# Kernel optimization log

Measured on AMD Instinct MI355X. Metric: run time of the kernel, lower is better.

Reference implementation:

```python
import jax, jax.numpy as jnp
import numpy as np

HIDDEN = 1024
HEADS = 16
HEAD_DIM = HIDDEN // HEADS  # 64


def setup_inputs() -> dict:
    key = jax.random.key(0)
    ks = jax.random.split(key, 5)
    B, S = 1, 4096
    inputs = jax.random.normal(ks[0], (B, S, HIDDEN), dtype=jnp.float32)
    # Xavier-uniform-ish init for square [out, in] weights (torch Linear layout)
    lim = float(np.sqrt(6.0 / (HIDDEN + HIDDEN)))
    def w(k):
        return jax.random.uniform(k, (HIDDEN, HIDDEN), jnp.float32, -lim, lim)
    return {
        "inputs": inputs,
        "Wq": w(ks[1]), "bq": jnp.zeros((HIDDEN,), jnp.float32),
        "Wk": w(ks[2]), "bk": jnp.zeros((HIDDEN,), jnp.float32),
        "Wv": w(ks[3]), "bv": jnp.zeros((HIDDEN,), jnp.float32),
        "Wo": w(ks[4]), "bo": jnp.zeros((HIDDEN,), jnp.float32),
    }


def reference(inputs, Wq, bq, Wk, bk, Wv, bv, Wo, bo):
    # Chunked online-softmax attention (causal_mask=False) is mathematically
    # identical to standard softmax multi-head attention.
    B, S, _ = inputs.shape
    def proj(W, b):
        # torch Linear: x @ W.T + b, then split heads -> [B, S, H, D]
        return (inputs @ W.T + b).reshape(B, S, HEADS, HEAD_DIM)
    q = proj(Wq, bq) / jnp.asarray(np.sqrt(HEAD_DIM), inputs.dtype)
    k = proj(Wk, bk)
    v = proj(Wv, bv)
    scores = jnp.einsum("bqhd,bkhd->bhqk", q, k)          # [B, H, S, S]
    attn = jax.nn.softmax(scores, axis=-1)
    ctx = jnp.einsum("bhqk,bkhd->bqhd", attn, v)           # [B, S, H, D]
    ctx = ctx.reshape(B, S, HIDDEN)
    return ctx @ Wo.T + bo
```

## Files before the change

### kernel.cpp

```cpp
#include <hip/hip_runtime.h>
#include <hip/hip_bf16.h>

typedef float f32x4 __attribute__((ext_vector_type(4)));
typedef float f32x16 __attribute__((ext_vector_type(16)));
typedef unsigned short u16x8 __attribute__((ext_vector_type(8)));
typedef unsigned int u32x2 __attribute__((ext_vector_type(2)));
typedef unsigned int u32x4 __attribute__((ext_vector_type(4)));
typedef __bf16 b16x8 __attribute__((ext_vector_type(8)));

static __device__ __forceinline__ unsigned short f2bf(float f) {
    unsigned int u = __builtin_bit_cast(unsigned int, f);
    return (unsigned short)((u + 0x7fffu + ((u >> 16) & 1u)) >> 16);
}

static __device__ __forceinline__ float bf2f(unsigned short u) {
    return __builtin_bit_cast(float, (unsigned int)u << 16);
}

static __device__ __forceinline__ unsigned int pkbf(float a, float b) {
    unsigned short x = __builtin_bit_cast(unsigned short, (__bf16)a);
    unsigned short y = __builtin_bit_cast(unsigned short, (__bf16)b);
    return (unsigned int)x | ((unsigned int)y << 16);
}

static __device__ __forceinline__ f32x4 mfma16(u16x8 a, u16x8 b, f32x4 c) {
    return __builtin_amdgcn_mfma_f32_16x16x32_bf16(
        __builtin_bit_cast(b16x8, a), __builtin_bit_cast(b16x8, b), c, 0, 0, 0);
}

static __device__ __forceinline__ f32x16 mfma32(u16x8 a, u16x8 b, f32x16 c) {
    return __builtin_amdgcn_mfma_f32_32x32x16_bf16(
        __builtin_bit_cast(b16x8, a), __builtin_bit_cast(b16x8, b), c, 0, 0, 0);
}

static __device__ __forceinline__ void gload16(const void* g, void* l) {
    __builtin_amdgcn_global_load_lds(
        (const __attribute__((address_space(1))) void*)g,
        (__attribute__((address_space(3))) void*)l, 16, 0, 0);
}

__global__ __launch_bounds__(256)
void convert_all(const float* __restrict__ x,
                 const float* __restrict__ wq, const float* __restrict__ wk,
                 const float* __restrict__ wv,
                 unsigned short* __restrict__ xb,
                 unsigned short* __restrict__ wqb, unsigned short* __restrict__ wkb,
                 unsigned short* __restrict__ wvb)
{
    const int bk = (int)blockIdx.x;
    const float* src;
    unsigned short* dst;
    int base;
    if (bk < 2048) { src = x; dst = xb; base = bk; }
    else {
        int wi = (bk - 2048) >> 9;
        src = (wi == 0) ? wq : (wi == 1) ? wk : wv;
        dst = (wi == 0) ? wqb : (wi == 1) ? wkb : wvb;
        base = (bk - 2048) & 511;
    }
    size_t i = ((size_t)base * 256 + threadIdx.x) * 8;
    f32x4 a = *reinterpret_cast<const f32x4*>(&src[i]);
    f32x4 b = *reinterpret_cast<const f32x4*>(&src[i + 4]);
    u16x8 r;
    r[0] = f2bf(a[0]); r[1] = f2bf(a[1]); r[2] = f2bf(a[2]); r[3] = f2bf(a[3]);
    r[4] = f2bf(b[0]); r[5] = f2bf(b[1]); r[6] = f2bf(b[2]); r[7] = f2bf(b[3]);
    *reinterpret_cast<u16x8*>(&dst[i]) = r;
}

__global__ __launch_bounds__(256)
void gemm_qkv(const unsigned short* __restrict__ A,
              const unsigned short* __restrict__ B0, const unsigned short* __restrict__ B1,
              const unsigned short* __restrict__ B2,
              const float* __restrict__ bias0, const float* __restrict__ bias1,
              const float* __restrict__ bias2,
              void* c0, void* c1, void* c2,
              int K, float scale0)
{
    __shared__ unsigned short As[128][32];
    __shared__ unsigned short Bs[128][32];
    const int t = (int)threadIdx.x;
    const int wave = t >> 6, lane = t & 63;
    const int wr = wave >> 1, wc = wave & 1;
    const int lo = lane & 15, g = lane >> 4;

    const int bid = (int)blockIdx.x;
    const int xc = bid & 7, c = bid >> 3;
    const int rowb = (xc >> 1) * 8 + (c & 7);
    const int colb = (xc & 1) * 12 + (c >> 3);
    const int brow = rowb * 128, bcol = colb * 128;
    const int w = bcol >> 10;
    const int segcol = bcol & 1023;
    const unsigned short* Bw = (w == 0) ? B0 : (w == 1) ? B1 : B2;
    const float* bi = (w == 0) ? bias0 : (w == 1) ? bias1 : bias2;
    const float scale = (w == 0) ? scale0 : 1.0f;

    const int glr = lane >> 2, glc = (lane & 3) * 8;

    f32x4 acc[4][4] = {};

    for (int kt = 0; kt < K; kt += 32) {
        __syncthreads();
        #pragma unroll
        for (int i = 0; i < 2; ++i) {
            int r = wave * 32 + i * 16;
            gload16(&A[(size_t)(brow + r + glr) * K + kt + glc], &As[r][0]);
            gload16(&Bw[(size_t)(segcol + r + glr) * K + kt + glc], &Bs[r][0]);
        }
        __syncthreads();

        u16x8 af[4], bf[4];
        #pragma unroll
        for (int mf = 0; mf < 4; ++mf)
            af[mf] = *reinterpret_cast<const u16x8*>(&As[wr * 64 + mf * 16 + lo][g * 8]);
        #pragma unroll
        for (int nf = 0; nf < 4; ++nf)
            bf[nf] = *reinterpret_cast<const u16x8*>(&Bs[wc * 64 + nf * 16 + lo][g * 8]);
        #pragma unroll
        for (int mf = 0; mf < 4; ++mf)
            #pragma unroll
            for (int nf = 0; nf < 4; ++nf)
                acc[mf][nf] = mfma16(af[mf], bf[nf], acc[mf][nf]);
    }

    void* cp = (w == 0) ? c0 : (w == 1) ? c1 : c2;
    #pragma unroll
    for (int nf = 0; nf < 4; ++nf) {
        int colLocal = wc * 64 + nf * 16 + lo;
        int cw = segcol + colLocal;
        float bv = bi[cw];
        if (w == 2) {
            #pragma unroll
            for (int mf = 0; mf < 4; ++mf) {
                int rowb2 = brow + wr * 64 + mf * 16 + g * 4;
                ushort4 u;
                u.x = f2bf(acc[mf][nf][0] + bv);
                u.y = f2bf(acc[mf][nf][1] + bv);
                u.z = f2bf(acc[mf][nf][2] + bv);
                u.w = f2bf(acc[mf][nf][3] + bv);
                *reinterpret_cast<ushort4*>(
                    &((unsigned short*)cp)[(size_t)cw * 4096 + rowb2]) = u;
            }
        } else {
            #pragma unroll
            for (int mf = 0; mf < 4; ++mf) {
                #pragma unroll
                for (int j = 0; j < 4; ++j) {
                    int row = brow + wr * 64 + mf * 16 + g * 4 + j;
                    ((unsigned short*)cp)[(size_t)row * 1024 + cw] =
                        f2bf((acc[mf][nf][j] + bv) * scale);
                }
            }
        }
    }
}

__global__ __launch_bounds__(256)
void gemm_o(const unsigned short* __restrict__ A, const unsigned short* __restrict__ Bw,
            const float* __restrict__ bi, float* __restrict__ cp, int K)
{
    __shared__ unsigned short As[128][32];
    __shared__ unsigned short Bs[64][32];
    const int t = (int)threadIdx.x;
    const int wave = t >> 6, lane = t & 63;
    const int wr = wave >> 1, wc = wave & 1;
    const int lo = lane & 15, g = lane >> 4;
    const int bid = (int)blockIdx.x;
    const int xc = bid & 7, c = bid >> 3;
    const int colb = (xc & 1) * 8 + (c & 7);
    const int rowb = (xc >> 1) * 8 + (c >> 3);
    const int brow = rowb * 128, bcol = colb * 64;

    const int row0 = t >> 2, c8 = t & 3;
    const int row1 = row0 + 64;

    f32x4 acc[4][2] = {};
    u16x8 aReg[2], bReg;

    aReg[0] = *reinterpret_cast<const u16x8*>(&A[(size_t)(brow + row0) * K + c8 * 8]);
    aReg[1] = *reinterpret_cast<const u16x8*>(&A[(size_t)(brow + row1) * K + c8 * 8]);
    bReg    = *reinterpret_cast<const u16x8*>(&Bw[(size_t)(bcol + row0) * K + c8 * 8]);

    for (int kt = 0; kt < K; kt += 32) {
        __syncthreads();
        *reinterpret_cast<u16x8*>(&As[row0][c8 * 8]) = aReg[0];
        *reinterpret_cast<u16x8*>(&As[row1][c8 * 8]) = aReg[1];
        *reinterpret_cast<u16x8*>(&Bs[row0][c8 * 8]) = bReg;
        __syncthreads();

        int ktn = kt + 32; if (ktn >= K) ktn = 0;
        aReg[0] = *reinterpret_cast<const u16x8*>(&A[(size_t)(brow + row0) * K + ktn + c8 * 8]);
        aReg[1] = *reinterpret_cast<const u16x8*>(&A[(size_t)(brow + row1) * K + ktn + c8 * 8]);
        bReg    = *reinterpret_cast<const u16x8*>(&Bw[(size_t)(bcol + row0) * K + ktn + c8 * 8]);

        u16x8 af[4], bf[2];
        #pragma unroll
        for (int mf = 0; mf < 4; ++mf)
            af[mf] = *reinterpret_cast<const u16x8*>(&As[wr * 64 + mf * 16 + lo][g * 8]);
        #pragma unroll
        for (int nf = 0; nf < 2; ++nf)
            bf[nf] = *reinterpret_cast<const u16x8*>(&Bs[wc * 32 + nf * 16 + lo][g * 8]);
        #pragma unroll
        for (int mf = 0; mf < 4; ++mf)
            #pragma unroll
            for (int nf = 0; nf < 2; ++nf)
                acc[mf][nf] = mfma16(af[mf], bf[nf], acc[mf][nf]);
    }

    #pragma unroll
    for (int nf = 0; nf < 2; ++nf) {
        int cw = bcol + wc * 32 + nf * 16 + lo;
        float bv = bi[cw];
        #pragma unroll
        for (int mf = 0; mf < 4; ++mf)
            #pragma unroll
            for (int j = 0; j < 4; ++j) {
                int row = brow + wr * 64 + mf * 16 + g * 4 + j;
                cp[(size_t)row * 1024 + cw] = acc[mf][nf][j] + bv;
            }
    }
}

template<int SPLIT>
__global__ __launch_bounds__(256, 2 * SPLIT)
void attn_kernel(const unsigned short* __restrict__ Q,
                 const unsigned short* __restrict__ Kg,
                 const unsigned short* __restrict__ VTg,
                 unsigned short* __restrict__ Ctx,
                 unsigned short* __restrict__ Opb, float* __restrict__ Lp)
{
    __shared__ unsigned short lds[2][2][4096];
    const int t = (int)threadIdx.x;
    const int lane = t & 63;
    const int q5 = lane & 31;
    const int hi = lane >> 5;
    const int bid = (int)blockIdx.x;
    const int sp = (SPLIT == 2) ? (bid >> 9) : 0;
    const int inner = bid & 511;
    const int h = (inner & 7) | (((inner >> 3) & 1) << 3);
    const int qb = inner >> 4;
    const int hc = h * 64;
    const int wv = t >> 6;
    const int qbase = qb * 128 + wv * 32;
    const int kt0 = sp * (4096 / SPLIT);
    const int NT = 4096 / (SPLIT * 64);

    const int sr = t >> 3, sch = t & 7;
    const int f0 = (sr ^ (sr >> 3)) & 7;
    const int scol0 = (sch ^ f0) * 8;
    const int scol1 = (sch ^ f0 ^ 4) * 8;
    const int sdst = sr * 64 + sch * 8;

    u16x8 qf[4];
    #pragma unroll
    for (int kf = 0; kf < 4; ++kf)
        qf[kf] = *reinterpret_cast<const u16x8*>(
            &Q[(size_t)(qbase + q5) * 1024 + hc + kf * 16 + hi * 8]);

    f32x16 o0 = {}, o1 = {};
    float lsum = 0.f;

    {
        u16x8 k0 = *reinterpret_cast<const u16x8*>(&Kg[(size_t)(kt0 + sr) * 1024 + hc + scol0]);
        u16x8 k1 = *reinterpret_cast<const u16x8*>(&Kg[(size_t)(kt0 + sr + 32) * 1024 + hc + scol1]);
        u16x8 v0 = *reinterpret_cast<const u16x8*>(&VTg[(size_t)(hc + sr) * 4096 + kt0 + scol0]);
        u16x8 v1 = *reinterpret_cast<const u16x8*>(&VTg[(size_t)(hc + sr + 32) * 4096 + kt0 + scol1]);
        *reinterpret_cast<u16x8*>(&lds[0][0][sdst]) = k0;
        *reinterpret_cast<u16x8*>(&lds[0][0][sdst + 2048]) = k1;
        *reinterpret_cast<u16x8*>(&lds[0][1][sdst]) = v0;
        *reinterpret_cast<u16x8*>(&lds[0][1][sdst + 2048]) = v1;
    }

    const int sz0 = (q5 ^ (q5 >> 3)) & 7;
    const int sz1 = sz0 ^ 4;
    int cur = 0;

    for (int tt = 0; tt < NT; ++tt) {
        __syncthreads();

        const int ktn = kt0 + (((tt + 1) & (NT - 1)) << 6);
        u16x8 kn0 = *reinterpret_cast<const u16x8*>(&Kg[(size_t)(ktn + sr) * 1024 + hc + scol0]);
        u16x8 kn1 = *reinterpret_cast<const u16x8*>(&Kg[(size_t)(ktn + sr + 32) * 1024 + hc + scol1]);
        u16x8 vn0 = *reinterpret_cast<const u16x8*>(&VTg[(size_t)(hc + sr) * 4096 + ktn + scol0]);
        u16x8 vn1 = *reinterpret_cast<const u16x8*>(&VTg[(size_t)(hc + sr + 32) * 4096 + ktn + scol1]);

        const unsigned short* Kb = lds[cur][0];
        const unsigned short* Vb = lds[cur][1];

        f32x16 s0 = {}, s1 = {};
        #pragma unroll
        for (int kf = 0; kf < 4; ++kf) {
            int off0 = ((kf * 2 + hi) ^ sz0) * 8;
            int off1 = ((kf * 2 + hi) ^ sz1) * 8;
            u16x8 ka0 = *reinterpret_cast<const u16x8*>(&Kb[q5 * 64 + off0]);
            u16x8 ka1 = *reinterpret_cast<const u16x8*>(&Kb[(q5 + 32) * 64 + off1]);
            s0 = mfma32(ka0, qf[kf], s0);
            s1 = mfma32(ka1, qf[kf], s1);
        }

        unsigned int u0[8], u1[8];
        float ps = 0.f;
        #pragma unroll
        for (int r = 0; r < 8; ++r) {
            float e0 = __builtin_amdgcn_exp2f(s0[2 * r]);
            float e1 = __builtin_amdgcn_exp2f(s0[2 * r + 1]);
            float e2 = __builtin_amdgcn_exp2f(s1[2 * r]);
            float e3 = __builtin_amdgcn_exp2f(s1[2 * r + 1]);
            ps += (e0 + e1) + (e2 + e3);
            u0[r] = pkbf(e0, e1);
            u1[r] = pkbf(e2, e3);
        }
        ps += __shfl_xor(ps, 32);
        lsum += ps;

        u16x8 pa[4];
        #pragma unroll
        for (int b = 0; b < 2; ++b) {
            #pragma unroll
            for (int ks = 0; ks < 2; ++ks) {
                unsigned int x0 = b ? u1[4 * ks]     : u0[4 * ks];
                unsigned int x1 = b ? u1[4 * ks + 1] : u0[4 * ks + 1];
                unsigned int y0 = b ? u1[4 * ks + 2] : u0[4 * ks + 2];
                unsigned int y1 = b ? u1[4 * ks + 3] : u0[4 * ks + 3];
                u32x2 r0 = __builtin_amdgcn_permlane32_swap(x0, y0, false, false);
                u32x2 r1 = __builtin_amdgcn_permlane32_swap(x1, y1, false, false);
                u32x4 d;
                d[0] = r0[0]; d[1] = r1[0]; d[2] = r0[1]; d[3] = r1[1];
                pa[2 * b + ks] = __builtin_bit_cast(u16x8, d);
            }
        }

        #pragma unroll
        for (int ks = 0; ks < 4; ++ks) {
            int off0 = ((ks * 2 + hi) ^ sz0) * 8;
            int off1 = ((ks * 2 + hi) ^ sz1) * 8;
            u16x8 vb0 = *reinterpret_cast<const u16x8*>(&Vb[q5 * 64 + off0]);
            u16x8 vb1 = *reinterpret_cast<const u16x8*>(&Vb[(q5 + 32) * 64 + off1]);
            o0 = mfma32(pa[ks], vb0, o0);
            o1 = mfma32(pa[ks], vb1, o1);
        }

        unsigned short* Kw = lds[cur ^ 1][0];
        unsigned short* Vw = lds[cur ^ 1][1];
        *reinterpret_cast<u16x8*>(&Kw[sdst]) = kn0;
        *reinterpret_cast<u16x8*>(&Kw[sdst + 2048]) = kn1;
        *reinterpret_cast<u16x8*>(&Vw[sdst]) = vn0;
        *reinterpret_cast<u16x8*>(&Vw[sdst + 2048]) = vn1;
        cur ^= 1;
    }

    if constexpr (SPLIT == 1) {
        float linv = 1.f / lsum;
        #pragma unroll
        for (int r = 0; r < 16; ++r) {
            int qr = (r & 3) + 8 * (r >> 2) + 4 * hi;
            float lr = __shfl(linv, qr);
            size_t row = (size_t)(qbase + qr) * 1024 + hc;
            Ctx[row + q5]      = f2bf(o0[r] * lr);
            Ctx[row + 32 + q5] = f2bf(o1[r] * lr);
        }
    } else {
        const int pb = (sp << 9) + (h * 32 + qb);
        unsigned short* op = Opb + ((size_t)pb * 128 + wv * 32) * 64;
        #pragma unroll
        for (int r = 0; r < 16; ++r) {
            int qr = (r & 3) + 8 * (r >> 2) + 4 * hi;
            op[(size_t)qr * 64 + q5]      = f2bf(o0[r]);
            op[(size_t)qr * 64 + 32 + q5] = f2bf(o1[r]);
        }
        if (hi == 0)
            Lp[(size_t)pb * 128 + wv * 32 + q5] = lsum;
    }
}

__global__ __launch_bounds__(256)
void combine2(const unsigned short* __restrict__ Opb, const float* __restrict__ Lp,
              unsigned short* __restrict__ Ctx,
              const float* __restrict__ Wo, unsigned short* __restrict__ wob)
{
    const int bk = (int)blockIdx.x;
    const int t = (int)threadIdx.x;
    if (bk >= 512) {
        size_t i = ((size_t)(bk - 512) * 256 + t) * 8;
        f32x4 a = *reinterpret_cast<const f32x4*>(&Wo[i]);
        f32x4 b = *reinterpret_cast<const f32x4*>(&Wo[i + 4]);
        u16x8 r;
        r[0] = f2bf(a[0]); r[1] = f2bf(a[1]); r[2] = f2bf(a[2]); r[3] = f2bf(a[3]);
        r[4] = f2bf(b[0]); r[5] = f2bf(b[1]); r[6] = f2bf(b[2]); r[7] = f2bf(b[3]);
        *reinterpret_cast<u16x8*>(&wob[i]) = r;
        return;
    }
    const int b = bk;
    const int h = b >> 5, qb = b & 31;
    const int r = t >> 1, dh = (t & 1) * 32;
    const size_t i0 = ((size_t)b * 128 + r) * 64 + dh;
    const size_t i1 = ((size_t)(512 + b) * 128 + r) * 64 + dh;
    const float l = Lp[(size_t)b * 128 + r] + Lp[(size_t)(512 + b) * 128 + r];
    const float inv = 1.f / l;
    const int row = qb * 128 + r;
    unsigned short* dst = &Ctx[(size_t)row * 1024 + h * 64 + dh];
    #pragma unroll
    for (int d = 0; d < 32; d += 8) {
        u16x8 a = *reinterpret_cast<const u16x8*>(&Opb[i0 + d]);
        u16x8 bq = *reinterpret_cast<const u16x8*>(&Opb[i1 + d]);
        u16x8 o;
        #pragma unroll
        for (int j = 0; j < 8; ++j)
            o[j] = f2bf((bf2f(a[j]) + bf2f(bq[j])) * inv);
        *reinterpret_cast<u16x8*>(&dst[d]) = o;
    }
}

extern "C" void kernel_launch(void* const* d_in, const int* in_sizes, int n_in,
                              void* d_out, int out_size, void* d_ws, size_t ws_size,
                              hipStream_t stream)
{
    const float* x  = (const float*)d_in[0];
    const float* Wq = (const float*)d_in[1];
    const float* bq = (const float*)d_in[2];
    const float* Wk = (const float*)d_in[3];
    const float* bk = (const float*)d_in[4];
    const float* Wv = (const float*)d_in[5];
    const float* bv = (const float*)d_in[6];
    const float* Wo = (const float*)d_in[7];
    const float* bo = (const float*)d_in[8];
    float* out = (float*)d_out;

    const int S = 4096, HID = 1024;
    const size_t MB = 1u << 20;
    unsigned short* xb  = (unsigned short*)d_ws;
    unsigned short* qws = xb + (size_t)S * HID;
    unsigned short* kws = qws + (size_t)S * HID;
    unsigned short* vtw = kws + (size_t)S * HID;
    unsigned short* cws = xb;
    unsigned short* Opb = (unsigned short*)((char*)d_ws + 32 * MB);
    float* Lp = (float*)((char*)d_ws + 64 * MB);
    unsigned short* wqb = (unsigned short*)((char*)d_ws + 32 * MB);
    unsigned short* wkb = wqb + (size_t)HID * HID;
    unsigned short* wvb = wkb + (size_t)HID * HID;
    unsigned short* wob = qws;

    const float qscale = 0.125f * 1.44269504088896f;

    convert_all<<<3584, 256, 0, stream>>>(x, Wq, Wk, Wv, xb, wqb, wkb, wvb);

    gemm_qkv<<<768, 256, 0, stream>>>(xb, wqb, wkb, wvb, bq, bk, bv,
                                      qws, kws, vtw, HID, qscale);

    attn_kernel<2><<<1024, 256, 0, stream>>>(qws, kws, vtw, cws, Opb, Lp);

    combine2<<<1024, 256, 0, stream>>>(Opb, Lp, cws, Wo, wob);

    gemm_o<<<512, 256, 0, stream>>>(cws, wob, bo, out, HID);
}
```

Before: 165.7 us.

## Process two query tiles per attention wave to reuse K/V fragments

Each attention block now handles 256 query rows (two 128-row sub-tiles A and B) instead of 128, so every K and V fragment loaded from LDS feeds twice as many MFMAs and global K/V traffic per query is halved. The grid drops from 1024 to 512 blocks, launch bounds go from 4 to 2 blocks per CU, and the partial-output layout and the combine kernel indexing change to match. In exchange, register pressure roughly doubles (four score and four output accumulators), which may cause spills or lower occupancy, and fewer blocks means less latency hiding across the GPU.

```diff
diff --git a/kernel.cpp b/kernel.cpp
--- a/kernel.cpp
+++ b/kernel.cpp
@@ -220,12 +220,10 @@
     }
 }
 
-template<int SPLIT>
-__global__ __launch_bounds__(256, 2 * SPLIT)
+__global__ __launch_bounds__(256, 2)
 void attn_kernel(const unsigned short* __restrict__ Q,
                  const unsigned short* __restrict__ Kg,
                  const unsigned short* __restrict__ VTg,
-                 unsigned short* __restrict__ Ctx,
                  unsigned short* __restrict__ Opb, float* __restrict__ Lp)
 {
     __shared__ unsigned short lds[2][2][4096];
@@ -234,15 +232,16 @@
     const int q5 = lane & 31;
     const int hi = lane >> 5;
     const int bid = (int)blockIdx.x;
-    const int sp = (SPLIT == 2) ? (bid >> 9) : 0;
-    const int inner = bid & 511;
+    const int sp = bid >> 8;
+    const int inner = bid & 255;
     const int h = (inner & 7) | (((inner >> 3) & 1) << 3);
     const int qb = inner >> 4;
     const int hc = h * 64;
     const int wv = t >> 6;
-    const int qbase = qb * 128 + wv * 32;
-    const int kt0 = sp * (4096 / SPLIT);
-    const int NT = 4096 / (SPLIT * 64);
+    const int qbaseA = qb * 256 + wv * 32;
+    const int qbaseB = qbaseA + 128;
+    const int kt0 = sp * 2048;
+    const int NT = 32;
 
     const int sr = t >> 3, sch = t & 7;
     const int f0 = (sr ^ (sr >> 3)) & 7;
@@ -250,14 +249,17 @@
     const int scol1 = (sch ^ f0 ^ 4) * 8;
     const int sdst = sr * 64 + sch * 8;
 
-    u16x8 qf[4];
+    u16x8 qfA[4], qfB[4];
     #pragma unroll
-    for (int kf = 0; kf < 4; ++kf)
-        qf[kf] = *reinterpret_cast<const u16x8*>(
-            &Q[(size_t)(qbase + q5) * 1024 + hc + kf * 16 + hi * 8]);
-
-    f32x16 o0 = {}, o1 = {};
-    float lsum = 0.f;
+    for (int kf = 0; kf < 4; ++kf) {
+        qfA[kf] = *reinterpret_cast<const u16x8*>(
+            &Q[(size_t)(qbaseA + q5) * 1024 + hc + kf * 16 + hi * 8]);
+        qfB[kf] = *reinterpret_cast<const u16x8*>(
+            &Q[(size_t)(qbaseB + q5) * 1024 + hc + kf * 16 + hi * 8]);
+    }
+
+    f32x16 oA0 = {}, oA1 = {}, oB0 = {}, oB1 = {};
+    float lsumA = 0.f, lsumB = 0.f;
 
     {
         u16x8 k0 = *reinterpret_cast<const u16x8*>(&Kg[(size_t)(kt0 + sr) * 1024 + hc + scol0]);
@@ -286,46 +288,73 @@
         const unsigned short* Kb = lds[cur][0];
         const unsigned short* Vb = lds[cur][1];
 
-        f32x16 s0 = {}, s1 = {};
+        f32x16 sA0 = {}, sA1 = {}, sB0 = {}, sB1 = {};
         #pragma unroll
         for (int kf = 0; kf < 4; ++kf) {
             int off0 = ((kf * 2 + hi) ^ sz0) * 8;
             int off1 = ((kf * 2 + hi) ^ sz1) * 8;
             u16x8 ka0 = *reinterpret_cast<const u16x8*>(&Kb[q5 * 64 + off0]);
             u16x8 ka1 = *reinterpret_cast<const u16x8*>(&Kb[(q5 + 32) * 64 + off1]);
-            s0 = mfma32(ka0, qf[kf], s0);
-            s1 = mfma32(ka1, qf[kf], s1);
-        }
-
-        unsigned int u0[8], u1[8];
-        float ps = 0.f;
+            sA0 = mfma32(ka0, qfA[kf], sA0);
+            sA1 = mfma32(ka1, qfA[kf], sA1);
+            sB0 = mfma32(ka0, qfB[kf], sB0);
+            sB1 = mfma32(ka1, qfB[kf], sB1);
+        }
+
+        unsigned int uA0[8], uA1[8], uB0[8], uB1[8];
+        float psA = 0.f, psB = 0.f;
         #pragma unroll
         for (int r = 0; r < 8; ++r) {
-            float e0 = __builtin_amdgcn_exp2f(s0[2 * r]);
-            float e1 = __builtin_amdgcn_exp2f(s0[2 * r + 1]);
-            float e2 = __builtin_amdgcn_exp2f(s1[2 * r]);
-            float e3 = __builtin_amdgcn_exp2f(s1[2 * r + 1]);
-            ps += (e0 + e1) + (e2 + e3);
-            u0[r] = pkbf(e0, e1);
-            u1[r] = pkbf(e2, e3);
-        }
-        ps += __shfl_xor(ps, 32);
-        lsum += ps;
-
-        u16x8 pa[4];
-        #pragma unroll
-        for (int b = 0; b < 2; ++b) {
+            float e0 = __builtin_amdgcn_exp2f(sA0[2 * r]);
+            float e1 = __builtin_amdgcn_exp2f(sA0[2 * r + 1]);
+            float e2 = __builtin_amdgcn_exp2f(sA1[2 * r]);
+            float e3 = __builtin_amdgcn_exp2f(sA1[2 * r + 1]);
+            psA += (e0 + e1) + (e2 + e3);
+            uA0[r] = pkbf(e0, e1);
+            uA1[r] = pkbf(e2, e3);
+        }
+        #pragma unroll
+        for (int r = 0; r < 8; ++r) {
+            float e0 = __builtin_amdgcn_exp2f(sB0[2 * r]);
+            float e1 = __builtin_amdgcn_exp2f(sB0[2 * r + 1]);
+            float e2 = __builtin_amdgcn_exp2f(sB1[2 * r]);
+            float e3 = __builtin_amdgcn_exp2f(sB1[2 * r + 1]);
+            psB += (e0 + e1) + (e2 + e3);
+            uB0[r] = pkbf(e0, e1);
+            uB1[r] = pkbf(e2, e3);
+        }
+        psA += __shfl_xor(psA, 32);
+        psB += __shfl_xor(psB, 32);
+        lsumA += psA;
+        lsumB += psB;
+
+        u16x8 paA[4], paB[4];
+        #pragma unroll
+        for (int b2 = 0; b2 < 2; ++b2) {
             #pragma unroll
             for (int ks = 0; ks < 2; ++ks) {
-                unsigned int x0 = b ? u1[4 * ks]     : u0[4 * ks];
-                unsigned int x1 = b ? u1[4 * ks + 1] : u0[4 * ks + 1];
-                unsigned int y0 = b ? u1[4 * ks + 2] : u0[4 * ks + 2];
-                unsigned int y1 = b ? u1[4 * ks + 3] : u0[4 * ks + 3];
-                u32x2 r0 = __builtin_amdgcn_permlane32_swap(x0, y0, false, false);
-                u32x2 r1 = __builtin_amdgcn_permlane32_swap(x1, y1, false, false);
-                u32x4 d;
-                d[0] = r0[0]; d[1] = r1[0]; d[2] = r0[1]; d[3] = r1[1];
-                pa[2 * b + ks] = __builtin_bit_cast(u16x8, d);
+                {
+                    unsigned int x0 = b2 ? uA1[4 * ks]     : uA0[4 * ks];
+                    unsigned int x1 = b2 ? uA1[4 * ks + 1] : uA0[4 * ks + 1];
+                    unsigned int y0 = b2 ? uA1[4 * ks + 2] : uA0[4 * ks + 2];
+                    unsigned int y1 = b2 ? uA1[4 * ks + 3] : uA0[4 * ks + 3];
+                    u32x2 r0 = __builtin_amdgcn_permlane32_swap(x0, y0, false, false);
+                    u32x2 r1 = __builtin_amdgcn_permlane32_swap(x1, y1, false, false);
+                    u32x4 d;
+                    d[0] = r0[0]; d[1] = r1[0]; d[2] = r0[1]; d[3] = r1[1];
+                    paA[2 * b2 + ks] = __builtin_bit_cast(u16x8, d);
+                }
+                {
+                    unsigned int x0 = b2 ? uB1[4 * ks]     : uB0[4 * ks];
+                    unsigned int x1 = b2 ? uB1[4 * ks + 1] : uB0[4 * ks + 1];
+                    unsigned int y0 = b2 ? uB1[4 * ks + 2] : uB0[4 * ks + 2];
+                    unsigned int y1 = b2 ? uB1[4 * ks + 3] : uB0[4 * ks + 3];
+                    u32x2 r0 = __builtin_amdgcn_permlane32_swap(x0, y0, false, false);
+                    u32x2 r1 = __builtin_amdgcn_permlane32_swap(x1, y1, false, false);
+                    u32x4 d;
+                    d[0] = r0[0]; d[1] = r1[0]; d[2] = r0[1]; d[3] = r1[1];
+                    paB[2 * b2 + ks] = __builtin_bit_cast(u16x8, d);
+                }
             }
         }
 
@@ -335,8 +364,10 @@
             int off1 = ((ks * 2 + hi) ^ sz1) * 8;
             u16x8 vb0 = *reinterpret_cast<const u16x8*>(&Vb[q5 * 64 + off0]);
             u16x8 vb1 = *reinterpret_cast<const u16x8*>(&Vb[(q5 + 32) * 64 + off1]);
-            o0 = mfma32(pa[ks], vb0, o0);
-            o1 = mfma32(pa[ks], vb1, o1);
+            oA0 = mfma32(paA[ks], vb0, oA0);
+            oA1 = mfma32(paA[ks], vb1, oA1);
+            oB0 = mfma32(paB[ks], vb0, oB0);
+            oB1 = mfma32(paB[ks], vb1, oB1);
         }
 
         unsigned short* Kw = lds[cur ^ 1][0];
@@ -348,27 +379,20 @@
         cur ^= 1;
     }
 
-    if constexpr (SPLIT == 1) {
-        float linv = 1.f / lsum;
-        #pragma unroll
-        for (int r = 0; r < 16; ++r) {
-            int qr = (r & 3) + 8 * (r >> 2) + 4 * hi;
-            float lr = __shfl(linv, qr);
-            size_t row = (size_t)(qbase + qr) * 1024 + hc;
-            Ctx[row + q5]      = f2bf(o0[r] * lr);
-            Ctx[row + 32 + q5] = f2bf(o1[r] * lr);
-        }
-    } else {
-        const int pb = (sp << 9) + (h * 32 + qb);
-        unsigned short* op = Opb + ((size_t)pb * 128 + wv * 32) * 64;
-        #pragma unroll
-        for (int r = 0; r < 16; ++r) {
-            int qr = (r & 3) + 8 * (r >> 2) + 4 * hi;
-            op[(size_t)qr * 64 + q5]      = f2bf(o0[r]);
-            op[(size_t)qr * 64 + 32 + q5] = f2bf(o1[r]);
-        }
-        if (hi == 0)
-            Lp[(size_t)pb * 128 + wv * 32 + q5] = lsum;
+    const int pb = (sp << 8) + (h * 16 + qb);
+    unsigned short* opA = Opb + ((size_t)pb * 256 + wv * 32) * 64;
+    unsigned short* opB = opA + (size_t)128 * 64;
+    #pragma unroll
+    for (int r = 0; r < 16; ++r) {
+        int qr = (r & 3) + 8 * (r >> 2) + 4 * hi;
+        opA[(size_t)qr * 64 + q5]      = f2bf(oA0[r]);
+        opA[(size_t)qr * 64 + 32 + q5] = f2bf(oA1[r]);
+        opB[(size_t)qr * 64 + q5]      = f2bf(oB0[r]);
+        opB[(size_t)qr * 64 + 32 + q5] = f2bf(oB1[r]);
+    }
+    if (hi == 0) {
+        Lp[(size_t)pb * 256 + wv * 32 + q5]       = lsumA;
+        Lp[(size_t)pb * 256 + 128 + wv * 32 + q5] = lsumB;
     }
 }
 
@@ -389,14 +413,15 @@
         *reinterpret_cast<u16x8*>(&wob[i]) = r;
         return;
     }
-    const int b = bk;
-    const int h = b >> 5, qb = b & 31;
+    const int pb = bk >> 1, half = bk & 1;
+    const int h = pb >> 4, qb = pb & 15;
     const int r = t >> 1, dh = (t & 1) * 32;
-    const size_t i0 = ((size_t)b * 128 + r) * 64 + dh;
-    const size_t i1 = ((size_t)(512 + b) * 128 + r) * 64 + dh;
-    const float l = Lp[(size_t)b * 128 + r] + Lp[(size_t)(512 + b) * 128 + r];
+    const int lrow = half * 128 + r;
+    const size_t i0 = ((size_t)pb * 256 + lrow) * 64 + dh;
+    const size_t i1 = ((size_t)(256 + pb) * 256 + lrow) * 64 + dh;
+    const float l = Lp[(size_t)pb * 256 + lrow] + Lp[(size_t)(256 + pb) * 256 + lrow];
     const float inv = 1.f / l;
-    const int row = qb * 128 + r;
+    const int row = qb * 256 + lrow;
     unsigned short* dst = &Ctx[(size_t)row * 1024 + h * 64 + dh];
     #pragma unroll
     for (int d = 0; d < 32; d += 8) {
@@ -446,7 +471,7 @@
     gemm_qkv<<<768, 256, 0, stream>>>(xb, wqb, wkb, wvb, bq, bk, bv,
                                       qws, kws, vtw, HID, qscale);
 
-    attn_kernel<2><<<1024, 256, 0, stream>>>(qws, kws, vtw, cws, Opb, Lp);
+    attn_kernel<<<512, 256, 0, stream>>>(qws, kws, vtw, Opb, Lp);
 
     combine2<<<1024, 256, 0, stream>>>(Opb, Lp, cws, Wo, wob);
 
```

Measured after the change: 158.7 us, median of 2. 4.3% less time.
